# Kernel optimization log

Measured on AMD Instinct MI355X. Metric: run time of the kernel, lower is better.

The kernel has to match this reference:

```python
import jax, jax.numpy as jnp
import numpy as np

NUM_GROUPS = 32
EPS = 1e-5


def setup_inputs() -> dict:
    key = jax.random.key(0)
    ks = jax.random.split(key, 6)
    B, C, H, W = 8, 128, 64, 64
    d = C // 8
    x = jax.random.normal(ks[0], (B, C, H, W), dtype=jnp.float32)
    # conv 1x1 weights stored as [out_ch, in_ch]; scaled like torch kaiming-uniform-ish
    s = 1.0 / np.sqrt(C)
    return {
        "x": x,
        "gn_w": jnp.ones((C,), jnp.float32),
        "gn_b": jnp.zeros((C,), jnp.float32),
        "q_w": jax.random.normal(ks[1], (d, C), jnp.float32) * s,
        "q_b": jnp.zeros((d,), jnp.float32),
        "k_w": jax.random.normal(ks[2], (d, C), jnp.float32) * s,
        "k_b": jnp.zeros((d,), jnp.float32),
        "v_w": jax.random.normal(ks[3], (C, C), jnp.float32) * s,
        "v_b": jnp.zeros((C,), jnp.float32),
        "p_w": jax.random.normal(ks[4], (C, C), jnp.float32) * s,
        "p_b": jnp.zeros((C,), jnp.float32),
    }


def _group_norm(x, w, b):
    B, C, H, W = x.shape
    g = NUM_GROUPS
    xr = x.reshape(B, g, C // g, H, W)
    mu = xr.mean(axis=(2, 3, 4), keepdims=True)
    var = xr.var(axis=(2, 3, 4), keepdims=True)
    xn = ((xr - mu) * jax.lax.rsqrt(var + EPS)).reshape(B, C, H, W)
    return xn * w[None, :, None, None] + b[None, :, None, None]


def reference(x, gn_w, gn_b, q_w, q_b, k_w, k_b, v_w, v_b, p_w, p_b):
    B, C, H, W = x.shape
    N = H * W
    h_ = _group_norm(x, gn_w, gn_b)            # [B,C,H,W]
    hf = h_.reshape(B, C, N)                   # flatten spatial
    # 1x1 convs == channel matmuls
    q = jnp.einsum('dc,bcn->bnd', q_w, hf) + q_b[None, None, :]   # [B,N,d]
    k = jnp.einsum('dc,bcn->bnd', k_w, hf) + k_b[None, None, :]   # [B,N,d]
    v = jnp.einsum('ec,bcn->ben', v_w, hf) + v_b[None, :, None]   # [B,C,N]
    d = q.shape[-1]
    scale = jnp.asarray(int(d) ** (-0.5), x.dtype)
    attn = jnp.einsum('bid,bjd->bij', q, k) * scale               # [B,N,N]
    attn = jax.nn.softmax(attn, axis=-1)
    a = jnp.einsum('bcj,bij->bci', v, attn)                       # [B,C,N]
    proj = jnp.einsum('ec,bcn->ben', p_w, a) + p_b[None, :, None]
    return x + proj.reshape(B, C, H, W)
```

## Files before the change

### kernel.cpp

```cpp
#include <hip/hip_runtime.h>
#include <math.h>


typedef short v8s __attribute__((ext_vector_type(8)));
typedef float v16f __attribute__((ext_vector_type(16)));

__device__ __forceinline__ unsigned short f2bf_rne(float f) {
  unsigned u = __float_as_uint(f);
  u += 0x7fffu + ((u >> 16) & 1u);
  return (unsigned short)(u >> 16);
}

__device__ __forceinline__ v8s mk8(unsigned a, unsigned b, unsigned c, unsigned d) {
  union { unsigned u[4]; v8s s; } x;
  x.u[0] = a; x.u[1] = b; x.u[2] = c; x.u[3] = d;
  return x.s;
}

__device__ __forceinline__ unsigned pack_trunc(float hi, float lo) {
  return __builtin_amdgcn_perm(__float_as_uint(hi), __float_as_uint(lo), 0x07060302u);
}

#define VT(b, n, c) (((((size_t)(b) * 256 + ((n) >> 4)) << 7) + (c)) * 16 + ((n) & 15))

#define WSB_MURS   0u
#define WSB_WCATB  4096u
#define WSB_BCAT   49152u
#define WSB_PWB    65536u
#define WSB_QBF    131072u
#define WSB_KBF    1310720u
#define WSB_VBF    2621440u

__global__ __launch_bounds__(512)
void gnprep_kernel(const float* __restrict__ x, float* __restrict__ mu_rs,
                   const float* __restrict__ qw, const float* __restrict__ qb,
                   const float* __restrict__ kw, const float* __restrict__ kb,
                   const float* __restrict__ vw, const float* __restrict__ vb,
                   const float* __restrict__ pw,
                   unsigned short* __restrict__ wcatb, float* __restrict__ bcat,
                   unsigned short* __restrict__ pwb) {
  const int id = blockIdx.x;
  {
    const float qs = 0.36067376022224085f;
    int idx = id * 512 + threadIdx.x;
    if (idx < 160 * 128) {
      int o = idx >> 7, c = idx & 127;
      float val;
      if (o < 16)       val = qw[o * 128 + c] * qs;
      else if (o < 32)  val = kw[(o - 16) * 128 + c];
      else              val = vw[(o - 32) * 128 + c];
      wcatb[idx] = f2bf_rne(val);
    } else if (idx < 160 * 128 + 160) {
      int o = idx - 160 * 128;
      bcat[o] = (o < 16) ? qb[o] * qs : (o < 32) ? kb[o - 16] : vb[o - 32];
    } else if (idx < 160 * 128 + 160 + 128 * 128) {
      int j = idx - (160 * 128 + 160);
      pwb[j] = f2bf_rne(pw[j]);
    }
  }
  const int bg = (id & 7) * 32 + (id >> 3);
  const float4* xp = (const float4*)(x + (size_t)bg * 16384);
  float s = 0.f, ss = 0.f;
#pragma unroll
  for (int u = 0; u < 8; ++u) {
    int i = threadIdx.x + u * 512;
    float4 v = xp[i];
    s  += v.x + v.y + v.z + v.w;
    ss += v.x * v.x + v.y * v.y + v.z * v.z + v.w * v.w;
  }
  for (int off = 32; off > 0; off >>= 1) {
    s  += __shfl_down(s, off, 64);
    ss += __shfl_down(ss, off, 64);
  }
  __shared__ float red[16];
  int lane = threadIdx.x & 63, wid = threadIdx.x >> 6;
  if (lane == 0) { red[wid * 2] = s; red[wid * 2 + 1] = ss; }
  __syncthreads();
  if (threadIdx.x == 0) {
    float S = 0.f, SS = 0.f;
    for (int w = 0; w < 8; ++w) { S += red[w * 2]; SS += red[w * 2 + 1]; }
    float mu  = S * (1.0f / 16384.0f);
    float var = SS * (1.0f / 16384.0f) - mu * mu;
    float rs  = rsqrtf(var + 1e-5f);
    mu_rs[bg * 2]     = mu;
    mu_rs[bg * 2 + 1] = rs;
  }
}

#define HS 136

__global__ __launch_bounds__(512)
void qkv_kernel(const float* __restrict__ x, const float* __restrict__ gnw,
                const float* __restrict__ gnb, const float* __restrict__ mu_rs,
                const unsigned short* __restrict__ wcatb, const float* __restrict__ bcat,
                unsigned short* __restrict__ qTb, unsigned short* __restrict__ kbf,
                unsigned short* __restrict__ vbf) {
  __shared__ alignas(16) unsigned short hs[64 * HS];
  __shared__ float scsh[128], shsh[128], bsh[160];
  const int id = blockIdx.x;
  const int b = id & 7, nb = (id >> 3) << 6;
  const int t = threadIdx.x;
  const int w = t >> 6, lane = t & 63, h = lane >> 5, l = lane & 31;
  const int nsub = w & 1, og = w >> 1;

  if (t < 128) {
    float mu = mu_rs[(b * 32 + (t >> 2)) * 2];
    float rs = mu_rs[(b * 32 + (t >> 2)) * 2 + 1];
    float gw = gnw[t], gb = gnb[t];
    scsh[t] = rs * gw; shsh[t] = gb - mu * rs * gw;
  }
  if (t < 160) bsh[t] = bcat[t];
  __syncthreads();

  const int sn = t & 63;
  const int c00 = (t >> 6) * 4;
  const float* xb = x + ((size_t)b * 128 << 12) + nb + sn;
#pragma unroll
  for (int it = 0; it < 4; ++it) {
    const int c0 = c00 + it * 32;
    float f0 = xb[(size_t)(c0)     << 12] * scsh[c0]     + shsh[c0];
    float f1 = xb[(size_t)(c0 + 1) << 12] * scsh[c0 + 1] + shsh[c0 + 1];
    float f2 = xb[(size_t)(c0 + 2) << 12] * scsh[c0 + 2] + shsh[c0 + 2];
    float f3 = xb[(size_t)(c0 + 3) << 12] * scsh[c0 + 3] + shsh[c0 + 3];
    uint2 u;
    u.x = (unsigned)f2bf_rne(f0) | ((unsigned)f2bf_rne(f1) << 16);
    u.y = (unsigned)f2bf_rne(f2) | ((unsigned)f2bf_rne(f3) << 16);
    *(uint2*)(&hs[sn * HS + c0]) = u;
  }
  __syncthreads();

  const int n = nb + nsub * 32 + l;
  const int otbase = (og == 0) ? 0 : og + 1;
  v16f acc[2];
#pragma unroll
  for (int a2 = 0; a2 < 2; ++a2)
#pragma unroll
    for (int r = 0; r < 16; ++r) acc[a2][r] = 0.f;

#pragma unroll
  for (int ks = 0; ks < 8; ++ks) {
    v8s bf = *(const v8s*)(&hs[(nsub * 32 + l) * HS + ks * 16 + 8 * h]);
    {
      v8s af = *(const v8s*)(wcatb + (otbase * 32 + l) * 128 + ks * 16 + 8 * h);
      acc[0] = __builtin_amdgcn_mfma_f32_32x32x16_bf16(af, bf, acc[0], 0, 0, 0);
    }
    if (og == 0) {
      v8s af = *(const v8s*)(wcatb + (32 + l) * 128 + ks * 16 + 8 * h);
      acc[1] = __builtin_amdgcn_mfma_f32_32x32x16_bf16(af, bf, acc[1], 0, 0, 0);
    }
  }

  if (og == 0) {
    const size_t nqk = ((size_t)b * 4096 + n) << 4;
#pragma unroll
    for (int r = 0; r < 16; ++r) {
      int o = 4 * h + (r & 3) + 8 * (r >> 2);
      unsigned short bv = f2bf_rne(acc[0][r] + bsh[o]);
      if (o < 16) qTb[((size_t)(b * 16 + o) << 12) + n] = bv;
      else        kbf[nqk + o - 16] = bv;
    }
#pragma unroll
    for (int r = 0; r < 16; ++r) {
      int o = 32 + 4 * h + (r & 3) + 8 * (r >> 2);
      vbf[VT(b, n, o - 32)] = f2bf_rne(acc[1][r] + bsh[o]);
    }
  } else {
#pragma unroll
    for (int r = 0; r < 16; ++r) {
      int o = otbase * 32 + 4 * h + (r & 3) + 8 * (r >> 2);
      vbf[VT(b, n, o - 32)] = f2bf_rne(acc[0][r] + bsh[o]);
    }
  }
}

#define OTS 136

__global__ __launch_bounds__(256)
void attn_kernel(const unsigned short* __restrict__ qTb,
                 const unsigned short* __restrict__ kbf,
                 const unsigned short* __restrict__ vbf,
                 const unsigned short* __restrict__ pwb,
                 const float* __restrict__ pb,
                 const float* __restrict__ x,
                 float* __restrict__ out) {
  __shared__ alignas(16) float ovs[9216];
  __shared__ float l_lds[64];
  __shared__ float pbs[128];

  const int id = blockIdx.x;
  const int b = id & 7, i0 = (id >> 3) << 6;
  const int t = threadIdx.x;
  const int w = t >> 6, lane = t & 63, h = lane >> 5, l = lane & 31;
  const int jsub = w & 1, ihalf = w >> 1;

  const unsigned short* kg = kbf + ((size_t)b << 16) + jsub * 512 + l * 16 + 8 * h;
  const unsigned short* vg = vbf + ((size_t)b << 19) + jsub * 4096 + l * 16 + 8 * h;

  if (t < 128) pbs[t] = pb[t];
  if (t < 64) l_lds[t] = 0.f;

  const int iglob = i0 + ihalf * 32 + l;
  unsigned qd[4];
#pragma unroll
  for (int e = 0; e < 4; ++e) {
    unsigned lo = qTb[((size_t)(b * 16 + 8 * h + 2 * e) << 12) + iglob];
    unsigned hi = qTb[((size_t)(b * 16 + 8 * h + 2 * e + 1) << 12) + iglob];
    qd[e] = lo | (hi << 16);
  }
  const v8s qf = mk8(qd[0], qd[1], qd[2], qd[3]);

  v16f zc;
#pragma unroll
  for (int r = 0; r < 16; ++r) zc[r] = 0.f;
  v16f acc[4];
#pragma unroll
  for (int ct = 0; ct < 4; ++ct)
#pragma unroll
    for (int r = 0; r < 16; ++r) acc[ct][r] = 0.f;
  float ls = 0.f;

  __syncthreads();

  v8s kf = *(const v8s*)kg;
  v8s vf[8];
#pragma unroll
  for (int ct = 0; ct < 4; ++ct) {
    vf[2 * ct]     = *(const v8s*)(vg + ct * 512);
    vf[2 * ct + 1] = *(const v8s*)(vg + 2048 + ct * 512);
  }

#pragma unroll 2
  for (int tile = 0; tile < 64; ++tile) {
    const int tn = (tile + 1) & 63;

    v8s kn = *(const v8s*)(kg + (size_t)tn * 1024);
    v8s vn[8];
    const unsigned short* vt = vg + (size_t)tn * 8192;
#pragma unroll
    for (int ct = 0; ct < 4; ++ct) {
      vn[2 * ct]     = *(const v8s*)(vt + ct * 512);
      vn[2 * ct + 1] = *(const v8s*)(vt + 2048 + ct * 512);
    }

    v16f st = __builtin_amdgcn_mfma_f32_32x32x16_bf16(kf, qf, zc, 0, 0, 0);
    float pe[16];
#pragma unroll
    for (int r = 0; r < 16; ++r) { pe[r] = __builtin_amdgcn_exp2f(st[r]); ls += pe[r]; }
    unsigned G[8];
#pragma unroll
    for (int g = 0; g < 4; ++g) {
      G[2 * g]     = pack_trunc(pe[4 * g + 1], pe[4 * g]);
      G[2 * g + 1] = pack_trunc(pe[4 * g + 3], pe[4 * g + 2]);
    }
    unsigned S0 = h ? G[0] : G[2], S1 = h ? G[1] : G[3];
    unsigned S2 = h ? G[4] : G[6], S3 = h ? G[5] : G[7];
    unsigned R0 = (unsigned)__shfl_xor((int)S0, 32, 64);
    unsigned R1 = (unsigned)__shfl_xor((int)S1, 32, 64);
    unsigned R2 = (unsigned)__shfl_xor((int)S2, 32, 64);
    unsigned R3 = (unsigned)__shfl_xor((int)S3, 32, 64);
    v8s pf0 = h ? mk8(R0, R1, G[2], G[3]) : mk8(G[0], G[1], R0, R1);
    v8s pf1 = h ? mk8(R2, R3, G[6], G[7]) : mk8(G[4], G[5], R2, R3);

#pragma unroll
    for (int ct = 0; ct < 4; ++ct) {
      acc[ct] = __builtin_amdgcn_mfma_f32_32x32x16_bf16(vf[2 * ct],     pf0, acc[ct], 0, 0, 0);
      acc[ct] = __builtin_amdgcn_mfma_f32_32x32x16_bf16(vf[2 * ct + 1], pf1, acc[ct], 0, 0, 0);
    }

    kf = kn;
#pragma unroll
    for (int u = 0; u < 8; ++u) vf[u] = vn[u];
  }

  atomicAdd(&l_lds[ihalf * 32 + l], ls);
  __syncthreads();

  float* const ov = ovs;
  if (jsub == 1) {
#pragma unroll
    for (int ct = 0; ct < 4; ++ct)
#pragma unroll
      for (int q = 0; q < 4; ++q) {
        float4 v4 = {acc[ct][4 * q], acc[ct][4 * q + 1],
                     acc[ct][4 * q + 2], acc[ct][4 * q + 3]};
        *(float4*)&ov[((ct * 2 + ihalf) * 32 + l) * 36 + 4 * h + 8 * q] = v4;
      }
  }
  __syncthreads();
  if (jsub == 0) {
#pragma unroll
    for (int ct = 0; ct < 4; ++ct)
#pragma unroll
      for (int q = 0; q < 4; ++q) {
        float4 v4 = *(float4*)&ov[((ct * 2 + ihalf) * 32 + l) * 36 + 4 * h + 8 * q];
        acc[ct][4 * q]     += v4.x;
        acc[ct][4 * q + 1] += v4.y;
        acc[ct][4 * q + 2] += v4.z;
        acc[ct][4 * q + 3] += v4.w;
      }
  }
  __syncthreads();

  unsigned short* const oT = (unsigned short*)ovs;
  if (jsub == 0) {
    const float li = 1.f / l_lds[ihalf * 32 + l];
    const int nrow = ihalf * 32 + l;
#pragma unroll
    for (int ct = 0; ct < 4; ++ct)
#pragma unroll
      for (int r = 0; r < 16; r += 2) {
        int c = ct * 32 + 4 * h + (r & 3) + 8 * (r >> 2);
        unsigned dw = (unsigned)f2bf_rne(acc[ct][r] * li) |
                      ((unsigned)f2bf_rne(acc[ct][r + 1] * li) << 16);
        *(unsigned*)(&oT[nrow * OTS + c]) = dw;
      }
  }
  __syncthreads();

#pragma unroll
  for (int nsub = 0; nsub < 2; ++nsub) {
    v16f a2;
#pragma unroll
    for (int r = 0; r < 16; ++r) a2[r] = 0.f;
#pragma unroll
    for (int ks = 0; ks < 8; ++ks) {
      v8s bf = *(const v8s*)(&oT[(nsub * 32 + l) * OTS + ks * 16 + 8 * h]);
      v8s af = *(const v8s*)(pwb + (w * 32 + l) * 128 + ks * 16 + 8 * h);
      a2 = __builtin_amdgcn_mfma_f32_32x32x16_bf16(af, bf, a2, 0, 0, 0);
    }
    const int n = i0 + nsub * 32 + l;
#pragma unroll
    for (int r = 0; r < 16; ++r) {
      int e = w * 32 + 4 * h + (r & 3) + 8 * (r >> 2);
      size_t idx = ((size_t)(b * 128 + e) << 12) + n;
      out[idx] = a2[r] + pbs[e] + x[idx];
    }
  }
}

extern "C" void kernel_launch(void* const* d_in, const int* in_sizes, int n_in,
                              void* d_out, int out_size, void* d_ws, size_t ws_size,
                              hipStream_t stream) {
  const float* x   = (const float*)d_in[0];
  const float* gnw = (const float*)d_in[1];
  const float* gnb = (const float*)d_in[2];
  const float* qw  = (const float*)d_in[3];
  const float* qb  = (const float*)d_in[4];
  const float* kw  = (const float*)d_in[5];
  const float* kb  = (const float*)d_in[6];
  const float* vw  = (const float*)d_in[7];
  const float* vb  = (const float*)d_in[8];
  const float* pw  = (const float*)d_in[9];
  const float* pb  = (const float*)d_in[10];
  float* out = (float*)d_out;
  char* ws = (char*)d_ws;

  float* mu_rs = (float*)(ws + WSB_MURS);
  unsigned short* wcatb = (unsigned short*)(ws + WSB_WCATB);
  float* bcat = (float*)(ws + WSB_BCAT);
  unsigned short* pwb = (unsigned short*)(ws + WSB_PWB);
  unsigned short* qTb = (unsigned short*)(ws + WSB_QBF);
  unsigned short* kbf = (unsigned short*)(ws + WSB_KBF);
  unsigned short* vbf = (unsigned short*)(ws + WSB_VBF);

  hipLaunchKernelGGL(gnprep_kernel, dim3(256), dim3(512), 0, stream,
                     x, mu_rs, qw, qb, kw, kb, vw, vb, pw, wcatb, bcat, pwb);
  hipLaunchKernelGGL(qkv_kernel, dim3(512), dim3(512), 0, stream,
                     x, gnw, gnb, mu_rs, wcatb, bcat, qTb, kbf, vbf);
  hipLaunchKernelGGL(attn_kernel, dim3(512), dim3(256), 0, stream,
                     qTb, kbf, vbf, pwb, pb, x, out);
}
```

Measured before the change: 153.2 us.

## Split attention over key halves with a separate combine and projection kernel

Splits the attention kernel's key loop in two, launching 1024 blocks instead of 512. Each block writes unnormalized fp32 partial outputs and row sums to workspace, and a new combine kernel sums the partials, normalizes, converts to bf16 and runs the output projection plus residual. The inner loop also swaps the shuffle-based half-wave exchange for v_permlane32_swap, raises wave priority around the MFMA block, and splits the row-sum accumulator into four chains. The aim is more parallelism on a GPU with many compute units, at the cost of an extra launch and roughly 33 MB of partial-result traffic.

New measurement: 165.5 us. 1.08x slower.

```diff
diff --git a/kernel.cpp b/kernel.cpp
--- a/kernel.cpp
+++ b/kernel.cpp
@@ -30,6 +30,8 @@
 #define WSB_QBF    131072u
 #define WSB_KBF    1310720u
 #define WSB_VBF    2621440u
+#define WSB_OPART  11010048u
+#define WSB_LPART  44564480u
 
 __global__ __launch_bounds__(512)
 void gnprep_kernel(const float* __restrict__ x, float* __restrict__ mu_rs,
@@ -173,22 +175,17 @@
   }
 }
 
-#define OTS 136
-
 __global__ __launch_bounds__(256)
 void attn_kernel(const unsigned short* __restrict__ qTb,
                  const unsigned short* __restrict__ kbf,
                  const unsigned short* __restrict__ vbf,
-                 const unsigned short* __restrict__ pwb,
-                 const float* __restrict__ pb,
-                 const float* __restrict__ x,
-                 float* __restrict__ out) {
+                 float* __restrict__ opart, float* __restrict__ lpart) {
   __shared__ alignas(16) float ovs[9216];
   __shared__ float l_lds[64];
-  __shared__ float pbs[128];
 
   const int id = blockIdx.x;
-  const int b = id & 7, i0 = (id >> 3) << 6;
+  const int b = id & 7, jh = (id >> 3) & 1, it = id >> 4;
+  const int i0 = it << 6;
   const int t = threadIdx.x;
   const int w = t >> 6, lane = t & 63, h = lane >> 5, l = lane & 31;
   const int jsub = w & 1, ihalf = w >> 1;
@@ -196,7 +193,6 @@
   const unsigned short* kg = kbf + ((size_t)b << 16) + jsub * 512 + l * 16 + 8 * h;
   const unsigned short* vg = vbf + ((size_t)b << 19) + jsub * 4096 + l * 16 + 8 * h;
 
-  if (t < 128) pbs[t] = pb[t];
   if (t < 64) l_lds[t] = 0.f;
 
   const int iglob = i0 + ihalf * 32 + l;
@@ -217,21 +213,25 @@
   for (int ct = 0; ct < 4; ++ct)
 #pragma unroll
     for (int r = 0; r < 16; ++r) acc[ct][r] = 0.f;
-  float ls = 0.f;
-
-  __syncthreads();
-
-  v8s kf = *(const v8s*)kg;
+  float ls0 = 0.f, ls1 = 0.f, ls2 = 0.f, ls3 = 0.f;
+
+  __syncthreads();
+
+  const int tb = jh << 5;
+  v8s kf = *(const v8s*)(kg + (size_t)tb * 1024);
   v8s vf[8];
-#pragma unroll
-  for (int ct = 0; ct < 4; ++ct) {
-    vf[2 * ct]     = *(const v8s*)(vg + ct * 512);
-    vf[2 * ct + 1] = *(const v8s*)(vg + 2048 + ct * 512);
+  {
+    const unsigned short* vp = vg + (size_t)tb * 8192;
+#pragma unroll
+    for (int ct = 0; ct < 4; ++ct) {
+      vf[2 * ct]     = *(const v8s*)(vp + ct * 512);
+      vf[2 * ct + 1] = *(const v8s*)(vp + 2048 + ct * 512);
+    }
   }
 
 #pragma unroll 2
-  for (int tile = 0; tile < 64; ++tile) {
-    const int tn = (tile + 1) & 63;
+  for (int tt = 0; tt < 32; ++tt) {
+    const int tn = tb + ((tt + 1) & 31);
 
     v8s kn = *(const v8s*)(kg + (size_t)tn * 1024);
     v8s vn[8];
@@ -245,34 +245,40 @@
     v16f st = __builtin_amdgcn_mfma_f32_32x32x16_bf16(kf, qf, zc, 0, 0, 0);
     float pe[16];
 #pragma unroll
-    for (int r = 0; r < 16; ++r) { pe[r] = __builtin_amdgcn_exp2f(st[r]); ls += pe[r]; }
+    for (int r = 0; r < 16; ++r) pe[r] = __builtin_amdgcn_exp2f(st[r]);
+    ls0 += pe[0] + pe[4] + pe[8]  + pe[12];
+    ls1 += pe[1] + pe[5] + pe[9]  + pe[13];
+    ls2 += pe[2] + pe[6] + pe[10] + pe[14];
+    ls3 += pe[3] + pe[7] + pe[11] + pe[15];
     unsigned G[8];
 #pragma unroll
     for (int g = 0; g < 4; ++g) {
       G[2 * g]     = pack_trunc(pe[4 * g + 1], pe[4 * g]);
       G[2 * g + 1] = pack_trunc(pe[4 * g + 3], pe[4 * g + 2]);
     }
-    unsigned S0 = h ? G[0] : G[2], S1 = h ? G[1] : G[3];
-    unsigned S2 = h ? G[4] : G[6], S3 = h ? G[5] : G[7];
-    unsigned R0 = (unsigned)__shfl_xor((int)S0, 32, 64);
-    unsigned R1 = (unsigned)__shfl_xor((int)S1, 32, 64);
-    unsigned R2 = (unsigned)__shfl_xor((int)S2, 32, 64);
-    unsigned R3 = (unsigned)__shfl_xor((int)S3, 32, 64);
-    v8s pf0 = h ? mk8(R0, R1, G[2], G[3]) : mk8(G[0], G[1], R0, R1);
-    v8s pf1 = h ? mk8(R2, R3, G[6], G[7]) : mk8(G[4], G[5], R2, R3);
-
+    unsigned A0 = G[0], B0 = G[2], A1 = G[1], B1 = G[3];
+    unsigned A2 = G[4], B2 = G[6], A3 = G[5], B3 = G[7];
+    asm("v_permlane32_swap_b32 %0, %1" : "+v"(A0), "+v"(B0));
+    asm("v_permlane32_swap_b32 %0, %1" : "+v"(A1), "+v"(B1));
+    asm("v_permlane32_swap_b32 %0, %1" : "+v"(A2), "+v"(B2));
+    asm("v_permlane32_swap_b32 %0, %1" : "+v"(A3), "+v"(B3));
+    v8s pf0 = mk8(A0, A1, B0, B1);
+    v8s pf1 = mk8(A2, A3, B2, B3);
+
+    __builtin_amdgcn_s_setprio(1);
 #pragma unroll
     for (int ct = 0; ct < 4; ++ct) {
       acc[ct] = __builtin_amdgcn_mfma_f32_32x32x16_bf16(vf[2 * ct],     pf0, acc[ct], 0, 0, 0);
       acc[ct] = __builtin_amdgcn_mfma_f32_32x32x16_bf16(vf[2 * ct + 1], pf1, acc[ct], 0, 0, 0);
     }
+    __builtin_amdgcn_s_setprio(0);
 
     kf = kn;
 #pragma unroll
     for (int u = 0; u < 8; ++u) vf[u] = vn[u];
   }
 
-  atomicAdd(&l_lds[ihalf * 32 + l], ls);
+  atomicAdd(&l_lds[ihalf * 32 + l], (ls0 + ls1) + (ls2 + ls3));
   __syncthreads();
 
   float* const ov = ovs;
@@ -287,33 +293,62 @@
       }
   }
   __syncthreads();
+  float* const opb = opart + ((size_t)id << 13);
   if (jsub == 0) {
+    const int row = ihalf * 32 + l;
 #pragma unroll
     for (int ct = 0; ct < 4; ++ct)
 #pragma unroll
       for (int q = 0; q < 4; ++q) {
         float4 v4 = *(float4*)&ov[((ct * 2 + ihalf) * 32 + l) * 36 + 4 * h + 8 * q];
-        acc[ct][4 * q]     += v4.x;
-        acc[ct][4 * q + 1] += v4.y;
-        acc[ct][4 * q + 2] += v4.z;
-        acc[ct][4 * q + 3] += v4.w;
+        v4.x += acc[ct][4 * q];
+        v4.y += acc[ct][4 * q + 1];
+        v4.z += acc[ct][4 * q + 2];
+        v4.w += acc[ct][4 * q + 3];
+        *(float4*)(opb + row * 128 + ct * 32 + 4 * h + 8 * q) = v4;
       }
   }
-  __syncthreads();
-
-  unsigned short* const oT = (unsigned short*)ovs;
-  if (jsub == 0) {
-    const float li = 1.f / l_lds[ihalf * 32 + l];
-    const int nrow = ihalf * 32 + l;
-#pragma unroll
-    for (int ct = 0; ct < 4; ++ct)
-#pragma unroll
-      for (int r = 0; r < 16; r += 2) {
-        int c = ct * 32 + 4 * h + (r & 3) + 8 * (r >> 2);
-        unsigned dw = (unsigned)f2bf_rne(acc[ct][r] * li) |
-                      ((unsigned)f2bf_rne(acc[ct][r + 1] * li) << 16);
-        *(unsigned*)(&oT[nrow * OTS + c]) = dw;
-      }
+  if (t < 64) lpart[((size_t)id << 6) + t] = l_lds[t];
+}
+
+#define OTS 136
+
+__global__ __launch_bounds__(256)
+void combine_kernel(const float* __restrict__ opart, const float* __restrict__ lpart,
+                    const unsigned short* __restrict__ pwb,
+                    const float* __restrict__ pb,
+                    const float* __restrict__ x,
+                    float* __restrict__ out) {
+  __shared__ alignas(16) unsigned short oT[64 * OTS];
+  __shared__ float pbs[128];
+
+  const int id = blockIdx.x;
+  const int b = id & 7, it = id >> 3, i0 = it << 6;
+  const int t = threadIdx.x;
+  const int w = t >> 6, lane = t & 63, h = lane >> 5, l = lane & 31;
+
+  if (t < 128) pbs[t] = pb[t];
+
+  const int id0 = (it << 4) + b;
+  const int id1 = (it << 4) + 8 + b;
+
+  {
+    const int row = t & 63, cg = t >> 6;
+    const float* p0 = opart + ((size_t)id0 << 13) + row * 128 + cg * 32;
+    const float* p1 = opart + ((size_t)id1 << 13) + row * 128 + cg * 32;
+    const float li = 1.f / (lpart[((size_t)id0 << 6) + row] +
+                            lpart[((size_t)id1 << 6) + row]);
+#pragma unroll
+    for (int cc = 0; cc < 8; ++cc) {
+      float4 a = *(const float4*)(p0 + cc * 4);
+      float4 c = *(const float4*)(p1 + cc * 4);
+      float s0 = (a.x + c.x) * li, s1 = (a.y + c.y) * li;
+      float s2 = (a.z + c.z) * li, s3 = (a.w + c.w) * li;
+      uint2 dw;
+      dw.x = (unsigned)f2bf_rne(s0) | ((unsigned)f2bf_rne(s1) << 16);
+      dw.y = (unsigned)f2bf_rne(s2) | ((unsigned)f2bf_rne(s3) << 16);
+      *(uint2*)(&oT[row * OTS + cg * 32 + cc * 4]) = dw;
+    }
   }
   __syncthreads();
 
@@ -362,11 +397,15 @@
   unsigned short* qTb = (unsigned short*)(ws + WSB_QBF);
   unsigned short* kbf = (unsigned short*)(ws + WSB_KBF);
   unsigned short* vbf = (unsigned short*)(ws + WSB_VBF);
+  float* opart = (float*)(ws + WSB_OPART);
+  float* lpart = (float*)(ws + WSB_LPART);
 
   hipLaunchKernelGGL(gnprep_kernel, dim3(256), dim3(512), 0, stream,
                      x, mu_rs, qw, qb, kw, kb, vw, vb, pw, wcatb, bcat, pwb);
   hipLaunchKernelGGL(qkv_kernel, dim3(512), dim3(512), 0, stream,
                      x, gnw, gnb, mu_rs, wcatb, bcat, qTb, kbf, vbf);
-  hipLaunchKernelGGL(attn_kernel, dim3(512), dim3(256), 0, stream,
-                     qTb, kbf, vbf, pwb, pb, x, out);
-}
+  hipLaunchKernelGGL(attn_kernel, dim3(1024), dim3(256), 0, stream,
+                     qTb, kbf, vbf, opart, lpart);
+  hipLaunchKernelGGL(combine_kernel, dim3(512), dim3(256), 0, stream,
+                     opart, lpart, pwb, pb, x, out);
+}
```
